# Optimization experiments

Hardware: AMD Instinct MI355X
Metric: run time of the kernel (lower is better)

## Reference

```python
import jax, jax.numpy as jnp
import numpy as np
from jax import lax


def _conv2d_same(x, w):
    # x: [B,Cin,H,W], w: [Cout,Cin,kh,kw], stride 1, SAME padding
    return lax.conv_general_dilated(x, w, (1, 1), 'SAME',
                                    dimension_numbers=('NCHW', 'OIHW', 'NCHW'))


def _descriptor(f_flat, w_a, b_a, w_aa, b_aa, w_m, b_m, w_mm, b_mm):
    # f_flat: [B,C,HW]; channel MLPs on avg/max pooled descriptors (1x1 convs == linear)
    avg = jnp.mean(f_flat, axis=-1)  # [B,C]
    mx = jnp.max(f_flat, axis=-1)    # [B,C]
    a = jax.nn.relu(avg @ w_a.T + b_a) @ w_aa.T + b_aa  # [B,C]
    m = jax.nn.relu(mx @ w_m.T + b_m) @ w_mm.T + b_mm   # [B,C]
    return a + m


def _spatial_gate(a_flat, b, c, h, w, conv1_w, conv1_b, conv2_w, conv2_b):
    a = a_flat.reshape(b, c, h, w)
    pooled = jnp.stack([jnp.mean(a, axis=1), jnp.max(a, axis=1)], axis=1)  # [B,2,H,W]
    y = jax.nn.relu(_conv2d_same(pooled, conv1_w) + conv1_b[None, :, None, None])
    y = _conv2d_same(y, conv2_w) + conv2_b[None, :, None, None]
    return jax.nn.softmax(y.reshape(b, 1, h * w), axis=-1)  # [B,1,HW]


def _cafm_forward(f1, f2,
                  w_avg1, b_avg1, w_max1, b_max1, w_avg11, b_avg11, w_max11, b_max11,
                  w_avg2, b_avg2, w_max2, b_max2, w_avg22, b_avg22, w_max22, b_max22,
                  conv1_w, conv1_b, conv2_w, conv2_b):
    b, c, h, w = f1.shape
    f1f = f1.reshape(b, c, h * w)
    f2f = f2.reshape(b, c, h * w)
    a1 = _descriptor(f1f, w_avg1, b_avg1, w_avg11, b_avg11, w_max1, b_max1, w_max11, b_max11)
    a2 = _descriptor(f2f, w_avg2, b_avg2, w_avg22, b_avg22, w_max2, b_max2, w_max22, b_max22)
    cross = jnp.einsum('bi,bj->bij', a1, a2)  # [B,C,C]
    at1 = jnp.einsum('bij,bjn->bin', jax.nn.softmax(cross, axis=-1), f1f)
    at2 = jnp.einsum('bij,bjn->bin', jax.nn.softmax(cross.transpose(0, 2, 1), axis=-1), f2f)
    g1 = _spatial_gate(at1, b, c, h, w, conv1_w, conv1_b, conv2_w, conv2_b)
    g2 = _spatial_gate(at2, b, c, h, w, conv1_w, conv1_b, conv2_w, conv2_b)
    o1 = (f1f * g1 + f1f).reshape(b, c, h, w)
    o2 = (f2f * g2 + f2f).reshape(b, c, h, w)
    return o1, o2


def setup_inputs() -> dict:
    key = jax.random.key(0)
    ks = jax.random.split(key, 24)
    B, C, H, W = 4, 64, 256, 256
    CR = 32  # reduction channels
    s = 0.05
    d = {
        'f1': jax.random.normal(ks[0], (B, C, H, W), jnp.float32),
        'f2': jax.random.normal(ks[1], (B, C, H, W), jnp.float32),
        'w_avg1': jax.random.normal(ks[2], (CR, C), jnp.float32) * s,
        'b_avg1': jnp.zeros((CR,), jnp.float32),
        'w_max1': jax.random.normal(ks[3], (CR, C), jnp.float32) * s,
        'b_max1': jnp.zeros((CR,), jnp.float32),
        'w_avg11': jax.random.normal(ks[4], (C, CR), jnp.float32) * s,
        'b_avg11': jnp.zeros((C,), jnp.float32),
        'w_max11': jax.random.normal(ks[5], (C, CR), jnp.float32) * s,
        'b_max11': jnp.zeros((C,), jnp.float32),
        'w_avg2': jax.random.normal(ks[6], (CR, C), jnp.float32) * s,
        'b_avg2': jnp.zeros((CR,), jnp.float32),
        'w_max2': jax.random.normal(ks[7], (CR, C), jnp.float32) * s,
        'b_max2': jnp.zeros((CR,), jnp.float32),
        'w_avg22': jax.random.normal(ks[8], (C, CR), jnp.float32) * s,
        'b_avg22': jnp.zeros((C,), jnp.float32),
        'w_max22': jax.random.normal(ks[9], (C, CR), jnp.float32) * s,
        'b_max22': jnp.zeros((C,), jnp.float32),
        'conv1_w': jax.random.normal(ks[10], (1, 2, 3, 3), jnp.float32) * s,
        'conv1_b': jnp.zeros((1,), jnp.float32),
        'conv2_w': jax.random.normal(ks[11], (1, 1, 3, 3), jnp.float32) * s,
        'conv2_b': jnp.zeros((1,), jnp.float32),
    }
    return d


def reference(f1, f2,
              w_avg1, b_avg1, w_max1, b_max1, w_avg11, b_avg11, w_max11, b_max11,
              w_avg2, b_avg2, w_max2, b_max2, w_avg22, b_avg22, w_max22, b_max22,
              conv1_w, conv1_b, conv2_w, conv2_b):
    return _cafm_forward(f1, f2,
                         w_avg1, b_avg1, w_max1, b_max1, w_avg11, b_avg11, w_max11, b_max11,
                         w_avg2, b_avg2, w_max2, b_max2, w_avg22, b_avg22, w_max22, b_max22,
                         conv1_w, conv1_b, conv2_w, conv2_b)
```

## Files before the change

kernel.cpp:

```cpp
#include <hip/hip_runtime.h>
#include <cstdint>

#define HW 65536

typedef __attribute__((ext_vector_type(8))) short bf16x8;
typedef __attribute__((ext_vector_type(4))) float f32x4;

#define D0 0
#define D1 4096
#define D2 4112
#define D3 8208
#define OFF_PS   12304
#define OFF_PM   13328
#define OFF_PB   14352
#define OFF_POOL 30736
#define OFF_BM   1079312
#define OFF_BS   1080336
#define OFF_Y    1081360

__device__ __forceinline__ unsigned short f2bf(float x) {
  union { float f; unsigned u; } v; v.f = x;
  unsigned r = v.u + 0x7fffu + ((v.u >> 16) & 1u);
  return (unsigned short)(r >> 16);
}

__device__ __forceinline__ void st_wt_f32(float* p, float v) {
  __hip_atomic_store(p, v, __ATOMIC_RELAXED, __HIP_MEMORY_SCOPE_AGENT);
}
__device__ __forceinline__ void st_wt_u32(unsigned* p, unsigned v) {
  __hip_atomic_store(p, v, __ATOMIC_RELAXED, __HIP_MEMORY_SCOPE_AGENT);
}

__device__ __forceinline__ void signal(unsigned* slot) {
  __syncthreads();
  if (threadIdx.x == 0) {
    asm volatile("s_waitcnt vmcnt(0)" ::: "memory");
    st_wt_u32(slot, 1u);
  }
}

__device__ __forceinline__ void wait_slots(const unsigned* fl, int idx, bool active) {
  bool ok;
  do {
    ok = true;
    if (active)
      ok = (__hip_atomic_load(fl + idx, __ATOMIC_RELAXED, __HIP_MEMORY_SCOPE_AGENT) != 0u);
    if (!ok) __builtin_amdgcn_s_sleep(8);
  } while (__syncthreads_and((int)ok) == 0);
  asm volatile("" ::: "memory");
}

__global__ __launch_bounds__(256, 4) void k_mega(
    const float* __restrict__ f1, const float* __restrict__ f2,
    float* __restrict__ ws, float* __restrict__ out,
    const float* __restrict__ w_avg1, const float* __restrict__ b_avg1,
    const float* __restrict__ w_max1, const float* __restrict__ b_max1,
    const float* __restrict__ w_avg11, const float* __restrict__ b_avg11,
    const float* __restrict__ w_max11, const float* __restrict__ b_max11,
    const float* __restrict__ w_avg2, const float* __restrict__ b_avg2,
    const float* __restrict__ w_max2, const float* __restrict__ b_max2,
    const float* __restrict__ w_avg22, const float* __restrict__ b_avg22,
    const float* __restrict__ w_max22, const float* __restrict__ b_max22,
    const float* __restrict__ cw1, const float* __restrict__ cb1,
    const float* __restrict__ cw2, const float* __restrict__ cb2) {

  __shared__ union {
    unsigned short tile[64 * 258];
    struct { float pl[2][20][36]; float t1l[18][34]; } cv;
    struct { float avg1[64], mx1[64], avg2[64], mx2[64],
             ha1[32], hm1[32], ha2[32], hm2[32],
             a1[64], a2[64], mm[4]; } mlp;
    float yst[512];
  } sm;
  __shared__ float red[8];

  unsigned* fl = (unsigned*)ws;
  const int tid = threadIdx.x;
  const int bx  = blockIdx.x;
  const int lane = tid & 63, wv = tid >> 6;

  {
    int ss = bx >> 7, ch = (bx >> 1) & 63, half = bx & 1;
    const float* fb = (ss >= 4) ? (f2 + ((size_t)(ss - 4) << 22))
                                : (f1 + ((size_t)ss << 22));
    const float4* p4 = (const float4*)(fb + (size_t)ch * HW + half * 32768);
    float sum = 0.f, mx = -3.4e38f;
#pragma unroll 8
    for (int it = 0; it < 32; ++it) {
      float4 v = p4[tid + (it << 8)];
      sum += (v.x + v.y) + (v.z + v.w);
      mx = fmaxf(mx, fmaxf(fmaxf(v.x, v.y), fmaxf(v.z, v.w)));
    }
    for (int o = 32; o > 0; o >>= 1) {
      sum += __shfl_down(sum, o);
      mx = fmaxf(mx, __shfl_down(mx, o));
    }
    if (lane == 0) { red[wv] = sum; red[4 + wv] = mx; }
    __syncthreads();
    if (tid == 0) {
      st_wt_f32(ws + OFF_PS + bx, red[0] + red[1] + red[2] + red[3]);
      st_wt_f32(ws + OFF_PM + bx, fmaxf(fmaxf(red[4], red[5]), fmaxf(red[6], red[7])));
    }
  }
  signal(fl + D0 + (bx << 2));

  if (bx < 4) {
    int b = bx;
    {
      int sidx = (tid < 128) ? ((b << 7) + tid) : (((4 + b) << 7) + (tid - 128));
      wait_slots(fl, D0 + (sidx << 2), true);
    }
    if (tid < 64) {
      int c = tid;
      sm.mlp.avg1[c] = (ws[OFF_PS + b * 128 + c * 2] + ws[OFF_PS + b * 128 + c * 2 + 1]) * (1.f / 65536.f);
      sm.mlp.mx1[c]  = fmaxf(ws[OFF_PM + b * 128 + c * 2], ws[OFF_PM + b * 128 + c * 2 + 1]);
      sm.mlp.avg2[c] = (ws[OFF_PS + (4 + b) * 128 + c * 2] + ws[OFF_PS + (4 + b) * 128 + c * 2 + 1]) * (1.f / 65536.f);
      sm.mlp.mx2[c]  = fmaxf(ws[OFF_PM + (4 + b) * 128 + c * 2], ws[OFF_PM + (4 + b) * 128 + c * 2 + 1]);
    }
    __syncthreads();
    if (tid < 32) {
      float s1 = b_avg1[tid], s2 = b_max1[tid], s3 = b_avg2[tid], s4 = b_max2[tid];
      for (int c = 0; c < 64; ++c) {
        s1 += w_avg1[tid * 64 + c] * sm.mlp.avg1[c];
        s2 += w_max1[tid * 64 + c] * sm.mlp.mx1[c];
        s3 += w_avg2[tid * 64 + c] * sm.mlp.avg2[c];
        s4 += w_max2[tid * 64 + c] * sm.mlp.mx2[c];
      }
      sm.mlp.ha1[tid] = fmaxf(s1, 0.f); sm.mlp.hm1[tid] = fmaxf(s2, 0.f);
      sm.mlp.ha2[tid] = fmaxf(s3, 0.f); sm.mlp.hm2[tid] = fmaxf(s4, 0.f);
    }
    __syncthreads();
    if (tid < 64) {
      float s1 = b_avg11[tid] + b_max11[tid];
      float s2 = b_avg22[tid] + b_max22[tid];
      for (int k = 0; k < 32; ++k) {
        s1 += w_avg11[tid * 32 + k] * sm.mlp.ha1[k] + w_max11[tid * 32 + k] * sm.mlp.hm1[k];
        s2 += w_avg22[tid * 32 + k] * sm.mlp.ha2[k] + w_max22[tid * 32 + k] * sm.mlp.hm2[k];
      }
      sm.mlp.a1[tid] = s1; sm.mlp.a2[tid] = s2;
    }
    __syncthreads();
    if (wv == 0) {
      float v = sm.mlp.a2[lane], mxv = v, mnv = v;
      for (int o = 32; o > 0; o >>= 1) {
        mxv = fmaxf(mxv, __shfl_xor(mxv, o));
        mnv = fminf(mnv, __shfl_xor(mnv, o));
      }
      if (lane == 0) { sm.mlp.mm[0] = mxv; sm.mlp.mm[1] = mnv; }
    } else if (wv == 1) {
      float v = sm.mlp.a1[lane], mxv = v, mnv = v;
      for (int o = 32; o > 0; o >>= 1) {
        mxv = fmaxf(mxv, __shfl_xor(mxv, o));
        mnv = fminf(mnv, __shfl_xor(mnv, o));
      }
      if (lane == 0) { sm.mlp.mm[2] = mxv; sm.mlp.mm[3] = mnv; }
    }
    __syncthreads();
    if (tid < 128) {
      int i = tid & 63;
      bool first = tid < 64;
      float s = first ? sm.mlp.a1[i] : sm.mlp.a2[i];
      const float* col = first ? sm.mlp.a2 : sm.mlp.a1;
      float m = (s >= 0.f) ? s * (first ? sm.mlp.mm[0] : sm.mlp.mm[2])
                           : s * (first ? sm.mlp.mm[1] : sm.mlp.mm[3]);
      float sum = 0.f;
      for (int j = 0; j < 64; ++j) sum += __expf(s * col[j] - m);
      float inv = 1.f / sum;
      int ssl = first ? b : (4 + b);
      unsigned* rowp = (unsigned*)(ws + OFF_PB) + (ssl << 11) + (i << 5);
      for (int jj = 0; jj < 32; ++jj) {
        unsigned lo = f2bf(__expf(s * col[2 * jj] - m) * inv);
        unsigned hi = f2bf(__expf(s * col[2 * jj + 1] - m) * inv);
        st_wt_u32(rowp + jj, lo | (hi << 16));
      }
    }
    signal(fl + D1 + (b << 2));
  }

  wait_slots(fl, D1 + ((tid & 3) << 2), tid < 4);

  {
    const unsigned short* Pb = (const unsigned short*)(ws + OFF_PB);
    const int c = lane & 15, q = lane >> 4;
    const int r0 = tid >> 6, cb = (tid & 63) << 2;
    for (int u = bx; u < 2048; u += 1024) {
      int ss = u >> 8, chunk = u & 255;
      int n0 = chunk << 8;
      const float* fb = (ss >= 4) ? (f2 + ((size_t)(ss - 4) << 22))
                                  : (f1 + ((size_t)ss << 22));
      __syncthreads();
#pragma unroll 4
      for (int i = 0; i < 16; ++i) {
        int row = (i << 2) + r0;
        float4 v = *(const float4*)(fb + (size_t)row * HW + n0 + cb);
        unsigned short* d = &sm.tile[row * 258 + cb];
        d[0] = f2bf(v.x); d[1] = f2bf(v.y); d[2] = f2bf(v.z); d[3] = f2bf(v.w);
      }
      __syncthreads();
      bf16x8 A[4][2];
#pragma unroll
      for (int mt = 0; mt < 4; ++mt)
#pragma unroll
        for (int s = 0; s < 2; ++s)
          A[mt][s] = *(const bf16x8*)(Pb + (ss << 12) + ((mt * 16 + c) << 6) + s * 32 + q * 8);
      float* poolp = ws + OFF_POOL + (size_t)ss * (2 * HW);
      int pxb = wv << 6;
#pragma unroll
      for (int nt = 0; nt < 4; ++nt) {
        int pcol = pxb + (nt << 4) + c;
        union { bf16x8 v; unsigned short s[8]; } u0, u1;
#pragma unroll
        for (int j = 0; j < 8; ++j) {
          u0.s[j] = sm.tile[(q * 8 + j) * 258 + pcol];
          u1.s[j] = sm.tile[(32 + q * 8 + j) * 258 + pcol];
        }
        f32x4 acc[4];
#pragma unroll
        for (int mt = 0; mt < 4; ++mt) {
          acc[mt] = (f32x4){0.f, 0.f, 0.f, 0.f};
          acc[mt] = __builtin_amdgcn_mfma_f32_16x16x32_bf16(A[mt][0], u0.v, acc[mt], 0, 0, 0);
          acc[mt] = __builtin_amdgcn_mfma_f32_16x16x32_bf16(A[mt][1], u1.v, acc[mt], 0, 0, 0);
        }
        float sum = 0.f, mxv = -3.4e38f;
#pragma unroll
        for (int mt = 0; mt < 4; ++mt)
#pragma unroll
          for (int r = 0; r < 4; ++r) {
            float v = acc[mt][r];
            sum += v;
            mxv = fmaxf(mxv, v);
          }
        sum += __shfl_xor(sum, 16);
        sum += __shfl_xor(sum, 32);
        mxv = fmaxf(mxv, __shfl_xor(mxv, 16));
        mxv = fmaxf(mxv, __shfl_xor(mxv, 32));
        int px = n0 + pcol;
        if (q == 0) st_wt_f32(poolp + px, sum * (1.f / 64.f));
        if (q == 1) st_wt_f32(poolp + HW + px, mxv);
      }
    }
  }
  signal(fl + D2 + (bx << 2));

  {
    int ss = bx >> 7, tile_id = bx & 127;
    int h0 = (tile_id >> 3) << 4;
    int w0 = (tile_id & 7) << 5;
    {
      int rr = h0 - 2 + tid;
      bool act = (tid < 20) && (rr >= 0) && (rr < 256);
      wait_slots(fl, D2 + ((((ss & 3) << 8) + rr) << 2), act);
    }
    const float* pp = ws + OFF_POOL + (size_t)ss * (2 * HW);
    float c1b = cb1[0], c2b = cb2[0];
    for (int i = tid; i < 1440; i += 256) {
      int ch = (i >= 720), rem = i - ch * 720;
      int rr = rem / 36, cc = rem - rr * 36;
      int h = h0 - 2 + rr, w = w0 - 2 + cc;
      float v = 0.f;
      if (h >= 0 && h < 256 && w >= 0 && w < 256) v = pp[ch * HW + (h << 8) + w];
      sm.cv.pl[ch][rr][cc] = v;
    }
    __syncthreads();
    for (int i = tid; i < 612; i += 256) {
      int rr = i / 34, cc = i - rr * 34;
      int h = h0 - 1 + rr, w = w0 - 1 + cc;
      float s = c1b;
#pragma unroll
      for (int ci = 0; ci < 2; ++ci)
#pragma unroll
        for (int kh = 0; kh < 3; ++kh)
#pragma unroll
          for (int kw = 0; kw < 3; ++kw)
            s += sm.cv.pl[ci][rr + kh][cc + kw] * cw1[ci * 9 + kh * 3 + kw];
      bool in = (h >= 0 && h < 256 && w >= 0 && w < 256);
      sm.cv.t1l[rr][cc] = in ? fmaxf(s, 0.f) : 0.f;
    }
    __syncthreads();
    float myy[2];
    float m = -3.4e38f;
#pragma unroll
    for (int k2 = 0; k2 < 2; ++k2) {
      int i = tid + (k2 << 8);
      int rr = i >> 5, cc = i & 31;
      float s = c2b;
#pragma unroll
      for (int kh = 0; kh < 3; ++kh)
#pragma unroll
        for (int kw = 0; kw < 3; ++kw)
          s += sm.cv.t1l[rr + kh][cc + kw] * cw2[kh * 3 + kw];
      st_wt_f32(ws + OFF_Y + (ss << 16) + ((h0 + rr) << 8) + w0 + cc, s);
      myy[k2] = s;
      m = fmaxf(m, s);
    }
    for (int o = 32; o > 0; o >>= 1) m = fmaxf(m, __shfl_xor(m, o));
    if (lane == 0) red[wv] = m;
    __syncthreads();
    float Mb = fmaxf(fmaxf(red[0], red[1]), fmaxf(red[2], red[3]));
    float z = __expf(myy[0] - Mb) + __expf(myy[1] - Mb);
    for (int o = 32; o > 0; o >>= 1) z += __shfl_xor(z, o);
    if (lane == 0) red[4 + wv] = z;
    __syncthreads();
    if (tid == 0) {
      st_wt_f32(ws + OFF_BM + bx, Mb);
      st_wt_f32(ws + OFF_BS + bx, red[4] + red[5] + red[6] + red[7]);
    }
  }
  signal(fl + D3 + (bx << 2));

  {
    int ss = bx >> 7, wq = bx & 127;
    wait_slots(fl, D3 + ((ss * 128 + (tid & 127)) << 2), tid < 128);
    float m = (tid < 128) ? ws[OFF_BM + ss * 128 + tid] : -3.4e38f;
    for (int o = 32; o > 0; o >>= 1) m = fmaxf(m, __shfl_xor(m, o));
    if (lane == 0) red[wv] = m;
    __syncthreads();
    float M = fmaxf(fmaxf(red[0], red[1]), fmaxf(red[2], red[3]));
    float z = (tid < 128) ? __expf(ws[OFF_BM + ss * 128 + tid] - M) * ws[OFF_BS + ss * 128 + tid] : 0.f;
    for (int o = 32; o > 0; o >>= 1) z += __shfl_xor(z, o);
    if (lane == 0) red[4 + wv] = z;
    __syncthreads();
    float iZ = 1.f / (red[4] + red[5] + red[6] + red[7]);
    int p0 = wq << 9;
    if (tid < 128) {
      float4 vy = *(const float4*)(ws + OFF_Y + (ss << 16) + p0 + (tid << 2));
      *(float4*)(&sm.yst[tid << 2]) = vy;
    }
    __syncthreads();
    const float* fsl = (ss >= 4) ? (f2 + ((size_t)(ss - 4) << 22))
                                 : (f1 + ((size_t)ss << 22));
    float* osl = out + ((size_t)ss << 22);
    int c0 = tid >> 7;
    int pxo = (tid & 127) << 2;
    float4 yv = *(const float4*)(&sm.yst[pxo]);
    float4 g;
    g.x = 1.f + __expf(yv.x - M) * iZ;
    g.y = 1.f + __expf(yv.y - M) * iZ;
    g.z = 1.f + __expf(yv.z - M) * iZ;
    g.w = 1.f + __expf(yv.w - M) * iZ;
#pragma unroll 8
    for (int i = 0; i < 32; ++i) {
      int ch = (i << 1) + c0;
      size_t gi = (size_t)ch * HW + p0 + pxo;
      float4 fv = *(const float4*)(fsl + gi);
      float4 o;
      o.x = fv.x * g.x; o.y = fv.y * g.y; o.z = fv.z * g.z; o.w = fv.w * g.w;
      *(float4*)(osl + gi) = o;
    }
  }
}

extern "C" void kernel_launch(void* const* d_in, const int* in_sizes, int n_in,
                              void* d_out, int out_size, void* d_ws, size_t ws_size,
                              hipStream_t stream) {
  const float* f1 = (const float*)d_in[0];
  const float* f2 = (const float*)d_in[1];
  const float* w_avg1  = (const float*)d_in[2];
  const float* b_avg1  = (const float*)d_in[3];
  const float* w_max1  = (const float*)d_in[4];
  const float* b_max1  = (const float*)d_in[5];
  const float* w_avg11 = (const float*)d_in[6];
  const float* b_avg11 = (const float*)d_in[7];
  const float* w_max11 = (const float*)d_in[8];
  const float* b_max11 = (const float*)d_in[9];
  const float* w_avg2  = (const float*)d_in[10];
  const float* b_avg2  = (const float*)d_in[11];
  const float* w_max2  = (const float*)d_in[12];
  const float* b_max2  = (const float*)d_in[13];
  const float* w_avg22 = (const float*)d_in[14];
  const float* b_avg22 = (const float*)d_in[15];
  const float* w_max22 = (const float*)d_in[16];
  const float* b_max22 = (const float*)d_in[17];
  const float* conv1_w = (const float*)d_in[18];
  const float* conv1_b = (const float*)d_in[19];
  const float* conv2_w = (const float*)d_in[20];
  const float* conv2_b = (const float*)d_in[21];
  float* ws = (float*)d_ws;
  float* out = (float*)d_out;

  hipMemsetAsync(d_ws, 0, 49216, stream);
  k_mega<<<1024, 256, 0, stream>>>(f1, f2, ws, out,
                                   w_avg1, b_avg1, w_max1, b_max1,
                                   w_avg11, b_avg11, w_max11, b_max11,
                                   w_avg2, b_avg2, w_max2, b_max2,
                                   w_avg22, b_avg22, w_max22, b_max22,
                                   conv1_w, conv1_b, conv2_w, conv2_b);
}
```

Measured before the change: 345.3 us.

## Fuse channel pooling with bf16 tile staging to reuse f1 tile in LDS

Phase 0 now has each block read the same 64x256 pixel tile of f1 and f2 that it later multiplies, computing per-row partial sums and maxes and keeping the f1 tile in LDS as bf16. The retained tile skips one global re-read in the attention-pooling phase. A new reduction stage across 128 blocks combines the partials before the MLP stage, which adds a flag level and more workspace. Blocks 0-3 re-stage f1 because the MLP stage overwrites the shared union, and bf16 conversion now uses the hip intrinsic.

After: 343.5 us. Within noise of the previous version (-0.5%).

```diff
diff --git a/kernel.cpp b/kernel.cpp
--- a/kernel.cpp
+++ b/kernel.cpp
@@ -1,4 +1,5 @@
 #include <hip/hip_runtime.h>
+#include <hip/hip_bf16.h>
 #include <cstdint>
 
 #define HW 65536
@@ -6,17 +7,21 @@
 typedef __attribute__((ext_vector_type(8))) short bf16x8;
 typedef __attribute__((ext_vector_type(4))) float f32x4;
 
-#define D0 0
-#define D1 4096
-#define D2 4112
-#define D3 8208
-#define OFF_PS   12304
-#define OFF_PM   13328
-#define OFF_PB   14352
-#define OFF_POOL 30736
-#define OFF_BM   1079312
-#define OFF_BS   1080336
-#define OFF_Y    1081360
+#define D0   0
+#define D1A  4096
+#define D1   4608
+#define D2   4624
+#define D3   8720
+#define FLAGS_BYTES 51264
+#define OFF_PARTS 12816
+#define OFF_PARTM 143888
+#define OFF_AVG   274960
+#define OFF_MXA   275472
+#define OFF_PB    275984
+#define OFF_POOL  292368
+#define OFF_BM    1340944
+#define OFF_BS    1341968
+#define OFF_Y     1342992
 
 __device__ __forceinline__ unsigned short f2bf(float x) {
   union { float f; unsigned u; } v; v.f = x;
@@ -48,6 +53,57 @@
     if (!ok) __builtin_amdgcn_s_sleep(8);
   } while (__syncthreads_and((int)ok) == 0);
   asm volatile("" ::: "memory");
+}
+
+__device__ __forceinline__ void stage_tile(const float* __restrict__ fb, int n0,
+                                           unsigned short* tile, int tid) {
+  int r0 = tid >> 6, cb = (tid & 63) << 2;
+#pragma unroll 4
+  for (int i = 0; i < 16; ++i) {
+    int row = (i << 2) + r0;
+    float4 v = *(const float4*)(fb + (size_t)row * HW + n0 + cb);
+    __hip_bfloat162 lo = __float22bfloat162_rn(make_float2(v.x, v.y));
+    __hip_bfloat162 hi = __float22bfloat162_rn(make_float2(v.z, v.w));
+    unsigned* d = (unsigned*)(tile + row * 258 + cb);
+    d[0] = *(unsigned*)&lo;
+    d[1] = *(unsigned*)&hi;
+  }
+}
+
+template <bool STORE>
+__device__ __forceinline__ void p0_tile(const float* __restrict__ fb, int n0, int ssp,
+                                        int chunk, unsigned short* tile,
+                                        float* __restrict__ ws, int lane, int wv) {
+  int ls = lane >> 4, lp = lane & 15;
+#pragma unroll
+  for (int rg = 0; rg < 4; ++rg) {
+    int row = (wv << 4) + (rg << 2) + ls;
+    const float4* rp = (const float4*)(fb + (size_t)row * HW + n0);
+    float sum = 0.f, mx = -3.4e38f;
+#pragma unroll
+    for (int i = 0; i < 4; ++i) {
+      int j = lp + (i << 4);
+      float4 v = rp[j];
+      sum += (v.x + v.y) + (v.z + v.w);
+      mx = fmaxf(mx, fmaxf(fmaxf(v.x, v.y), fmaxf(v.z, v.w)));
+      if (STORE) {
+        __hip_bfloat162 lo = __float22bfloat162_rn(make_float2(v.x, v.y));
+        __hip_bfloat162 hi = __float22bfloat162_rn(make_float2(v.z, v.w));
+        unsigned* d = (unsigned*)(tile + row * 258 + (j << 2));
+        d[0] = *(unsigned*)&lo;
+        d[1] = *(unsigned*)&hi;
+      }
+    }
+#pragma unroll
+    for (int o = 1; o < 16; o <<= 1) {
+      sum += __shfl_xor(sum, o);
+      mx = fmaxf(mx, __shfl_xor(mx, o));
+    }
+    if (lp == 0) {
+      st_wt_f32(ws + OFF_PARTS + (((ssp << 6) + row) << 8) + chunk, sum);
+      st_wt_f32(ws + OFF_PARTM + (((ssp << 6) + row) << 8) + chunk, mx);
+    }
+  }
 }
 
 __global__ __launch_bounds__(256, 4) void k_mega(
@@ -79,43 +135,44 @@
   const int bx  = blockIdx.x;
   const int lane = tid & 63, wv = tid >> 6;
 
-  {
-    int ss = bx >> 7, ch = (bx >> 1) & 63, half = bx & 1;
-    const float* fb = (ss >= 4) ? (f2 + ((size_t)(ss - 4) << 22))
-                                : (f1 + ((size_t)ss << 22));
-    const float4* p4 = (const float4*)(fb + (size_t)ch * HW + half * 32768);
-    float sum = 0.f, mx = -3.4e38f;
-#pragma unroll 8
-    for (int it = 0; it < 32; ++it) {
-      float4 v = p4[tid + (it << 8)];
-      sum += (v.x + v.y) + (v.z + v.w);
-      mx = fmaxf(mx, fmaxf(fmaxf(v.x, v.y), fmaxf(v.z, v.w)));
-    }
+  const int ss1 = bx >> 8, chunk = bx & 255, n0 = chunk << 8;
+  const float* fb1 = f1 + ((size_t)ss1 << 22);
+  const float* fb2 = f2 + ((size_t)ss1 << 22);
+
+  p0_tile<true >(fb1, n0, ss1,     chunk, sm.tile, ws, lane, wv);
+  p0_tile<false>(fb2, n0, ss1 + 4, chunk, sm.tile, ws, lane, wv);
+  signal(fl + D0 + (bx << 2));
+
+  if (bx < 128) {
+    int ssx = bx >> 4;
+    wait_slots(fl, D0 + ((((ssx & 3) << 8) | tid) << 2), true);
+    int r = (bx << 2) + wv;
+    float4 s4 = *(const float4*)(ws + OFF_PARTS + (r << 8) + (lane << 2));
+    float4 m4 = *(const float4*)(ws + OFF_PARTM + (r << 8) + (lane << 2));
+    float s = (s4.x + s4.y) + (s4.z + s4.w);
+    float m = fmaxf(fmaxf(m4.x, m4.y), fmaxf(m4.z, m4.w));
     for (int o = 32; o > 0; o >>= 1) {
-      sum += __shfl_down(sum, o);
-      mx = fmaxf(mx, __shfl_down(mx, o));
-    }
-    if (lane == 0) { red[wv] = sum; red[4 + wv] = mx; }
-    __syncthreads();
-    if (tid == 0) {
-      st_wt_f32(ws + OFF_PS + bx, red[0] + red[1] + red[2] + red[3]);
-      st_wt_f32(ws + OFF_PM + bx, fmaxf(fmaxf(red[4], red[5]), fmaxf(red[6], red[7])));
-    }
-  }
-  signal(fl + D0 + (bx << 2));
+      s += __shfl_xor(s, o);
+      m = fmaxf(m, __shfl_xor(m, o));
+    }
+    if (lane == 0) {
+      st_wt_f32(ws + OFF_AVG + r, s * (1.f / 65536.f));
+      st_wt_f32(ws + OFF_MXA + r, m);
+    }
+    signal(fl + D1A + (bx << 2));
+  }
 
   if (bx < 4) {
     int b = bx;
     {
-      int sidx = (tid < 128) ? ((b << 7) + tid) : (((4 + b) << 7) + (tid - 128));
-      wait_slots(fl, D0 + (sidx << 2), true);
+      int fidx = (tid < 16) ? (b * 16 + tid) : ((b + 4) * 16 + (tid - 16));
+      wait_slots(fl, D1A + (fidx << 2), tid < 32);
     }
     if (tid < 64) {
-      int c = tid;
-      sm.mlp.avg1[c] = (ws[OFF_PS + b * 128 + c * 2] + ws[OFF_PS + b * 128 + c * 2 + 1]) * (1.f / 65536.f);
-      sm.mlp.mx1[c]  = fmaxf(ws[OFF_PM + b * 128 + c * 2], ws[OFF_PM + b * 128 + c * 2 + 1]);
-      sm.mlp.avg2[c] = (ws[OFF_PS + (4 + b) * 128 + c * 2] + ws[OFF_PS + (4 + b) * 128 + c * 2 + 1]) * (1.f / 65536.f);
-      sm.mlp.mx2[c]  = fmaxf(ws[OFF_PM + (4 + b) * 128 + c * 2], ws[OFF_PM + (4 + b) * 128 + c * 2 + 1]);
+      sm.mlp.avg1[tid] = ws[OFF_AVG + (b << 6) + tid];
+      sm.mlp.mx1[tid]  = ws[OFF_MXA + (b << 6) + tid];
+      sm.mlp.avg2[tid] = ws[OFF_AVG + ((b + 4) << 6) + tid];
+      sm.mlp.mx2[tid]  = ws[OFF_MXA + ((b + 4) << 6) + tid];
     }
     __syncthreads();
     if (tid < 32) {
@@ -177,34 +234,22 @@
     signal(fl + D1 + (b << 2));
   }
 
-  wait_slots(fl, D1 + ((tid & 3) << 2), tid < 4);
+  wait_slots(fl, D1 + (ss1 << 2), tid == 0);
 
   {
-    const unsigned short* Pb = (const unsigned short*)(ws + OFF_PB);
+    const unsigned short* Pb16 = (const unsigned short*)(ws + OFF_PB);
     const int c = lane & 15, q = lane >> 4;
-    const int r0 = tid >> 6, cb = (tid & 63) << 2;
-    for (int u = bx; u < 2048; u += 1024) {
-      int ss = u >> 8, chunk = u & 255;
-      int n0 = chunk << 8;
-      const float* fb = (ss >= 4) ? (f2 + ((size_t)(ss - 4) << 22))
-                                  : (f1 + ((size_t)ss << 22));
-      __syncthreads();
-#pragma unroll 4
-      for (int i = 0; i < 16; ++i) {
-        int row = (i << 2) + r0;
-        float4 v = *(const float4*)(fb + (size_t)row * HW + n0 + cb);
-        unsigned short* d = &sm.tile[row * 258 + cb];
-        d[0] = f2bf(v.x); d[1] = f2bf(v.y); d[2] = f2bf(v.z); d[3] = f2bf(v.w);
-      }
-      __syncthreads();
+    const int pxb = wv << 6;
+
+    auto mfma_tile = [&](int ss) {
       bf16x8 A[4][2];
+      const unsigned short* Prow = Pb16 + (ss << 12);
 #pragma unroll
       for (int mt = 0; mt < 4; ++mt)
 #pragma unroll
         for (int s = 0; s < 2; ++s)
-          A[mt][s] = *(const bf16x8*)(Pb + (ss << 12) + ((mt * 16 + c) << 6) + s * 32 + q * 8);
+          A[mt][s] = *(const bf16x8*)(Prow + ((mt * 16 + c) << 6) + s * 32 + q * 8);
       float* poolp = ws + OFF_POOL + (size_t)ss * (2 * HW);
-      int pxb = wv << 6;
 #pragma unroll
       for (int nt = 0; nt < 4; ++nt) {
         int pcol = pxb + (nt << 4) + c;
@@ -238,7 +283,18 @@
         if (q == 0) st_wt_f32(poolp + px, sum * (1.f / 64.f));
         if (q == 1) st_wt_f32(poolp + HW + px, mxv);
       }
-    }
+    };
+
+    if (bx < 4) {
+      __syncthreads();
+      stage_tile(fb1, n0, sm.tile, tid);
+      __syncthreads();
+    }
+    mfma_tile(ss1);
+    __syncthreads();
+    stage_tile(fb2, n0, sm.tile, tid);
+    __syncthreads();
+    mfma_tile(ss1 + 4);
   }
   signal(fl + D2 + (bx << 2));
 
@@ -378,7 +434,7 @@
   float* ws = (float*)d_ws;
   float* out = (float*)d_out;
 
-  hipMemsetAsync(d_ws, 0, 49216, stream);
+  hipMemsetAsync(d_ws, 0, FLAGS_BYTES, stream);
   k_mega<<<1024, 256, 0, stream>>>(f1, f2, ws, out,
                                    w_avg1, b_avg1, w_max1, b_max1,
                                    w_avg11, b_avg11, w_max11, b_max11,
```
